# Optimization experiments

Measured on AMD Instinct MI355X. Metric: run time of the kernel, lower is better.

Reference implementation:

```python
import jax, jax.numpy as jnp
import numpy as np

NUM_HEADS = 12
KSIZE = 3
PAD = 1


def setup_inputs() -> dict:
    key = jax.random.key(0)
    ks = jax.random.split(key, 5)
    B, H, W, C = 4, 96, 96, 192
    x = jax.random.normal(ks[0], (B, H * W, C), jnp.float32)
    Wq = jax.random.normal(ks[1], (W, W), jnp.float32) * 0.02
    bq = jnp.zeros((W,), jnp.float32)
    Wkv = jax.random.normal(ks[2], (2 * W, W), jnp.float32) * 0.02
    bkv = jnp.zeros((2 * W,), jnp.float32)
    Wp = jax.random.normal(ks[3], (C, C), jnp.float32) * 0.02
    bp = jnp.zeros((C,), jnp.float32)
    f_qr = jnp.float32(1.0)
    f_kr = jnp.float32(1.0)
    f_vr = jnp.float32(1.0)
    return {"x": x, "Wq": Wq, "bq": bq, "Wkv": Wkv, "bkv": bkv, "Wp": Wp,
            "bp": bp, "f_qr": f_qr, "f_kr": f_kr, "f_vr": f_vr, "H": H, "W": W}


def reference(x, Wq, bq, Wkv, bkv, Wp, bp, f_qr, f_kr, f_vr, H, W):
    B, N, C = x.shape
    nh = NUM_HEADS
    hc = C // nh
    scale = C ** (-0.5)
    # faithful to torch: raw reshape of (B, N, C) into (B, C, H, W)
    xn = x.reshape(B, C, H, W)
    # q_proj is Linear over the last (width) axis, size Hw == W
    q = jnp.einsum('bchw,vw->bchv', xn, Wq) + bq            # (B,C,H,W)
    q = q.reshape(B, H, W, nh, hc).transpose(0, 3, 1, 2, 4)  # (B,nh,H,W,hc)
    q = (q * scale * f_qr).reshape(B, nh, H * W, hc)         # (B,nh,L,hc)
    # kv_proj: Linear(W -> 2W) over last axis
    kv = jnp.einsum('bchw,vw->bchv', xn, Wkv) + bkv          # (B,C,H,2W)
    kv = kv.reshape(B, H, W, 2, nh, hc).transpose(3, 0, 4, 5, 1, 2)  # (2,B,nh,hc,H,W)
    kv = jnp.pad(kv, ((0, 0),) * 4 + ((PAD, PAD), (PAD, PAD)))       # zero-pad spatial
    # unfold: 3x3 sliding windows, stride 1 -> one window per pixel
    patches = jnp.stack([kv[..., i:i + H, j:j + W]
                         for i in range(KSIZE) for j in range(KSIZE)], axis=4)
    # (2,B,nh,hc,9,H,W) -> (2,B,nh,L,9,hc); kernel index = kh*3+kw matches nn.Unfold
    patches = patches.reshape(2, B, nh, hc, KSIZE * KSIZE, H * W).transpose(0, 1, 2, 5, 4, 3)
    k = patches[0] * f_kr                                    # (B,nh,L,9,hc)
    v = patches[1] * f_vr
    attn = jax.nn.softmax(jnp.einsum('bnlc,bnlkc->bnlk', q, k), axis=-1)  # (B,nh,L,9)
    out = jnp.einsum('bnlk,bnlkc->bnlc', attn, v)            # (B,nh,L,hc)
    out = out.transpose(0, 2, 1, 3).reshape(B, H, W, C)      # (B,H,W,C)
    out = jnp.einsum('bhwc,oc->bhwo', out, Wp) + bp          # proj Linear(dim,dim)
    return out.reshape(B, H * W, C)
```

## Files before the change

kernel.cpp:

```cpp
#include <hip/hip_runtime.h>

#define HW2   96
#define NH    12
#define LPIX  (HW2*HW2)
#define BATCH 4

typedef __attribute__((ext_vector_type(8))) short bf16x8;
typedef __attribute__((ext_vector_type(4))) float f32x4;

static __device__ __forceinline__ float bf2f(unsigned short u) {
  union { unsigned int i; float f; } v; v.i = ((unsigned int)u) << 16; return v.f;
}
static __device__ __forceinline__ unsigned short f2bf(float f) {
  union { float f; unsigned int i; } v; v.f = f;
  unsigned int r = v.i + 0x7FFF + ((v.i >> 16) & 1);
  return (unsigned short)(r >> 16);
}

__global__ __launch_bounds__(256) void cvt_w_kernel(
    const float* __restrict__ Wq, const float* __restrict__ Wkv,
    const float* __restrict__ Wp,
    unsigned short* __restrict__ wqb, unsigned short* __restrict__ wkvb,
    unsigned short* __restrict__ wpb) {
  int i = blockIdx.x * 256 + threadIdx.x;
  if (i < 9216)       wqb[i]          = f2bf(Wq[i]);
  else if (i < 27648) wkvb[i - 9216]  = f2bf(Wkv[i - 9216]);
  else if (i < 64512) wpb[i - 27648]  = f2bf(Wp[i - 27648]);
}

__global__ __launch_bounds__(256) void qkv_gemm(
    const float* __restrict__ X,
    const unsigned short* __restrict__ wq, const unsigned short* __restrict__ wkv,
    const float* __restrict__ bq, const float* __restrict__ bkv,
    const float* __restrict__ fqr, const float* __restrict__ fkr,
    const float* __restrict__ fvr,
    unsigned short* __restrict__ Qb, unsigned short* __restrict__ KVb)
{
  __shared__ unsigned short lds[19456];
  unsigned short* xs  = lds;
  unsigned short* qo  = lds;
  unsigned short* kvo = lds + 6656;

  const int tid = threadIdx.x;
  const int r0  = blockIdx.x * 64;

  const float4* xsrc = (const float4*)(X + (size_t)r0 * 96);
  #pragma unroll
  for (int it = 0; it < 6; it++) {
    int c = tid + it * 256;
    float4 v = xsrc[c];
    int row = c / 24, col = (c % 24) * 4;
    ushort4 p;
    p.x = f2bf(v.x); p.y = f2bf(v.y); p.z = f2bf(v.z); p.w = f2bf(v.w);
    *(ushort4*)&xs[row * 120 + col] = p;
  }
  __syncthreads();

  const int lane = tid & 63, w = tid >> 6;
  const int col  = lane & 15;
  const int koff = (lane >> 4) * 8;
  const int arow = 16 * w + (lane & 15);
  const int rloc = 16 * w + 4 * (lane >> 4);

  bf16x8 af0 = *(const bf16x8*)&xs[arow * 120 + koff];
  bf16x8 af1 = *(const bf16x8*)&xs[arow * 120 + koff + 32];
  bf16x8 af2 = *(const bf16x8*)&xs[arow * 120 + koff + 64];
  __syncthreads();

  const float fqr0 = fqr[0] * 0.07216878364870322f;
  const float fkr0 = fkr[0], fvr0 = fvr[0];

  #pragma unroll
  for (int nt = 0; nt < 18; nt++) {
    const unsigned short* wrow = (nt < 6)
        ? wq  + (size_t)(nt * 16 + col) * 96 + koff
        : wkv + (size_t)((nt - 6) * 16 + col) * 96 + koff;
    bf16x8 b0 = *(const bf16x8*)(wrow);
    bf16x8 b1 = *(const bf16x8*)(wrow + 32);
    bf16x8 b2 = *(const bf16x8*)(wrow + 64);
    f32x4 acc = {0.f, 0.f, 0.f, 0.f};
    acc = __builtin_amdgcn_mfma_f32_16x16x32_bf16(af0, b0, acc, 0, 0, 0);
    acc = __builtin_amdgcn_mfma_f32_16x16x32_bf16(af1, b1, acc, 0, 0, 0);
    acc = __builtin_amdgcn_mfma_f32_16x16x32_bf16(af2, b2, acc, 0, 0, 0);

    if (nt < 6) {
      int u = nt * 16 + col;
      float bias = bq[u];
      #pragma unroll
      for (int i = 0; i < 4; i++)
        qo[(rloc + i) * 104 + u] = f2bf((acc[i] + bias) * fqr0);
    } else {
      int u = (nt - 6) * 16 + col;
      float bias = bkv[u];
      #pragma unroll
      for (int i = 0; i < 4; i++) {
        float s = (i & 1) ? fvr0 : fkr0;
        kvo[(rloc + i) * 200 + u] = f2bf((acc[i] + bias) * s);
      }
    }
  }
  __syncthreads();

  #pragma unroll
  for (int it = 0; it < 3; it++) {
    int c = tid + it * 256;
    int row = c / 12, cc = (c % 12) * 8;
    *(bf16x8*)(Qb + (size_t)(r0 + row) * 96 + cc) = *(const bf16x8*)&qo[row * 104 + cc];
  }
  #pragma unroll
  for (int it = 0; it < 6; it++) {
    int c = tid + it * 256;
    int row = c / 24, cc = (c % 24) * 8;
    *(bf16x8*)(KVb + (size_t)(r0 + row) * 192 + cc) = *(const bf16x8*)&kvo[row * 200 + cc];
  }
}

__global__ __launch_bounds__(384) void attnproj_kernel(
    const unsigned short* __restrict__ Qb, const unsigned short* __restrict__ KVb,
    const unsigned short* __restrict__ wp, const float* __restrict__ bp,
    float* __restrict__ Out)
{
  __shared__ unsigned short s_out[32 * 200];
  const int tid = threadIdx.x;
  const int bl0 = blockIdx.x * 32;

  {
    const int n  = tid % NH;
    const int pl = tid / NH;
    const int bl = bl0 + pl;
    const int l  = bl % LPIX;
    const int b  = bl / LPIX;
    const int h2 = l / HW2, w2 = l - h2 * HW2;

    const unsigned short* qp = Qb + (size_t)bl * 192 + n * 16;
    uint4 qA = *(const uint4*)(qp);
    uint4 qB = *(const uint4*)(qp + 8);

    const unsigned short* kvb = KVb + (size_t)b * (LPIX * 384) + n * 16;

    int  nbo[9];
    bool okk[9];
    uint4 kA[9], kB[9];
    #pragma unroll
    for (int kk = 0; kk < 9; kk++) {
      int hh = h2 + kk / 3 - 1;
      int ww = w2 + kk % 3 - 1;
      okk[kk] = ((unsigned)hh < (unsigned)HW2) && ((unsigned)ww < (unsigned)HW2);
      int hc = min(max(hh, 0), HW2 - 1);
      int wc = min(max(ww, 0), HW2 - 1);
      nbo[kk] = (hc * HW2 + wc) * 384;
      const unsigned short* kp = kvb + nbo[kk];
      kA[kk] = *(const uint4*)(kp);
      kB[kk] = *(const uint4*)(kp + 8);
    }

    float q[16];
    {
      const unsigned short* qs = (const unsigned short*)&qA;
      #pragma unroll
      for (int j = 0; j < 8; j++) q[j] = bf2f(qs[j]);
      qs = (const unsigned short*)&qB;
      #pragma unroll
      for (int j = 0; j < 8; j++) q[8 + j] = bf2f(qs[j]);
    }

    float sc[9];
    #pragma unroll
    for (int kk = 0; kk < 9; kk++) {
      float s = 0.f;
      const unsigned short* kd = (const unsigned short*)&kA[kk];
      #pragma unroll
      for (int j = 0; j < 8; j++) s = fmaf(q[j], bf2f(kd[j]), s);
      kd = (const unsigned short*)&kB[kk];
      #pragma unroll
      for (int j = 0; j < 8; j++) s = fmaf(q[8 + j], bf2f(kd[j]), s);
      sc[kk] = okk[kk] ? s : 0.f;
    }

    uint4 vA[9], vB[9];
    #pragma unroll
    for (int kk = 0; kk < 9; kk++) {
      const unsigned short* vp = kvb + nbo[kk] + 192;
      vA[kk] = *(const uint4*)(vp);
      vB[kk] = *(const uint4*)(vp + 8);
    }

    float m = sc[0];
    #pragma unroll
    for (int kk = 1; kk < 9; kk++) m = fmaxf(m, sc[kk]);
    float ssum = 0.f;
    #pragma unroll
    for (int kk = 0; kk < 9; kk++) {
      float e = __expf(sc[kk] - m);
      sc[kk] = e;
      ssum += e;
    }

    float acc[16];
    #pragma unroll
    for (int j = 0; j < 16; j++) acc[j] = 0.f;
    #pragma unroll
    for (int kk = 0; kk < 9; kk++) {
      float wgt = okk[kk] ? sc[kk] : 0.f;
      const unsigned short* vd = (const unsigned short*)&vA[kk];
      #pragma unroll
      for (int j = 0; j < 8; j++) acc[j] = fmaf(wgt, bf2f(vd[j]), acc[j]);
      vd = (const unsigned short*)&vB[kk];
      #pragma unroll
      for (int j = 0; j < 8; j++) acc[8 + j] = fmaf(wgt, bf2f(vd[j]), acc[8 + j]);
    }
    float rinv = 1.f / ssum;
    unsigned short od[16];
    #pragma unroll
    for (int j = 0; j < 16; j++) od[j] = f2bf(acc[j] * rinv);
    unsigned short* op = s_out + pl * 200 + n * 16;
    *(uint4*)(op)     = *(uint4*)&od[0];
    *(uint4*)(op + 8) = *(uint4*)&od[8];
  }
  __syncthreads();

  const int lane = tid & 63, w = tid >> 6;
  const int wr = w & 1, wh = w >> 1;
  const int col  = lane & 15;
  const int koff = (lane >> 4) * 8;
  const int arow = 16 * wr + (lane & 15);
  const int rbase = bl0 + 16 * wr + 4 * (lane >> 4);

  bf16x8 af[6];
  #pragma unroll
  for (int kt = 0; kt < 6; kt++)
    af[kt] = *(const bf16x8*)&s_out[arow * 200 + koff + kt * 32];

  #pragma unroll
  for (int t4 = 0; t4 < 4; t4++) {
    int nt = wh * 4 + t4;
    const unsigned short* wrow = wp + (size_t)(nt * 16 + col) * 192 + koff;
    f32x4 acc = {0.f, 0.f, 0.f, 0.f};
    #pragma unroll
    for (int kt = 0; kt < 6; kt++) {
      bf16x8 bfr = *(const bf16x8*)(wrow + kt * 32);
      acc = __builtin_amdgcn_mfma_f32_16x16x32_bf16(af[kt], bfr, acc, 0, 0, 0);
    }
    int u = nt * 16 + col;
    float bias = bp[u];
    #pragma unroll
    for (int i = 0; i < 4; i++)
      Out[(size_t)(rbase + i) * 192 + u] = acc[i] + bias;
  }
}

extern "C" void kernel_launch(void* const* d_in, const int* in_sizes, int n_in,
                              void* d_out, int out_size, void* d_ws, size_t ws_size,
                              hipStream_t stream) {
  const float* x   = (const float*)d_in[0];
  const float* Wq  = (const float*)d_in[1];
  const float* bq  = (const float*)d_in[2];
  const float* Wkv = (const float*)d_in[3];
  const float* bkv = (const float*)d_in[4];
  const float* Wp  = (const float*)d_in[5];
  const float* bp  = (const float*)d_in[6];
  const float* fqr = (const float*)d_in[7];
  const float* fkr = (const float*)d_in[8];
  const float* fvr = (const float*)d_in[9];

  char* ws = (char*)d_ws;
  unsigned short* Qb   = (unsigned short*)ws;
  unsigned short* KVb  = (unsigned short*)(ws + 14155776);
  unsigned short* wqb  = (unsigned short*)(ws + 42467328);
  unsigned short* wkvb = (unsigned short*)(ws + 42485760);
  unsigned short* wpb  = (unsigned short*)(ws + 42522624);

  cvt_w_kernel<<<dim3(252), dim3(256), 0, stream>>>(Wq, Wkv, Wp, wqb, wkvb, wpb);

  qkv_gemm<<<dim3(1152), dim3(256), 0, stream>>>(
      x, wqb, wkvb, bq, bkv, fqr, fkr, fvr, Qb, KVb);

  attnproj_kernel<<<dim3(1152), dim3(384), 0, stream>>>(
      Qb, KVb, wpb, bp, (float*)d_out);
}
```

Before: 77.32 us.

## Store Q and KV head-major so attention gathers are contiguous per head

The QKV GEMM epilogue now writes Q and K/V into head-major buffers (batch, head, pixel, channels), with K and V for each pixel interleaved into 32-element rows. The attention kernel maps threads so the 32 pixels in a block share one head, which makes each 3x3 neighbour gather a short contiguous read within that head's plane instead of a 768-byte strided access across all heads. The LDS row stride for the projection input is padded to avoid bank conflicts. The cost is scattered 16-byte stores in the GEMM epilogue.

```diff
diff --git a/kernel.cpp b/kernel.cpp
--- a/kernel.cpp
+++ b/kernel.cpp
@@ -34,7 +34,7 @@
     const float* __restrict__ bq, const float* __restrict__ bkv,
     const float* __restrict__ fqr, const float* __restrict__ fkr,
     const float* __restrict__ fvr,
-    unsigned short* __restrict__ Qb, unsigned short* __restrict__ KVb)
+    unsigned short* __restrict__ Qh, unsigned short* __restrict__ KVh)
 {
   __shared__ unsigned short lds[19456];
   unsigned short* xs  = lds;
@@ -43,6 +43,8 @@
 
   const int tid = threadIdx.x;
   const int r0  = blockIdx.x * 64;
+  const int b   = r0 / 18432;
+  const int lb  = (r0 % 18432) >> 1;
 
   const float4* xsrc = (const float4*)(X + (size_t)r0 * 96);
   #pragma unroll
@@ -103,40 +105,52 @@
 
   #pragma unroll
   for (int it = 0; it < 3; it++) {
-    int c = tid + it * 256;
-    int row = c / 12, cc = (c % 12) * 8;
-    *(bf16x8*)(Qb + (size_t)(r0 + row) * 96 + cc) = *(const bf16x8*)&qo[row * 104 + cc];
+    int m = tid + it * 256;
+    int n = m >> 6, rem = m & 63;
+    int l_loc = rem >> 1, half = (m & 1) * 8;
+    int srow = 2 * l_loc + (n >= 6);
+    int scol = (n % 6) * 16 + half;
+    unsigned short* dst = Qh + (size_t)b * 1769472 + (size_t)n * 147456
+                        + (size_t)(lb + l_loc) * 16 + half;
+    *(uint4*)dst = *(const uint4*)&qo[srow * 104 + scol];
   }
   #pragma unroll
   for (int it = 0; it < 6; it++) {
-    int c = tid + it * 256;
-    int row = c / 24, cc = (c % 24) * 8;
-    *(bf16x8*)(KVb + (size_t)(r0 + row) * 192 + cc) = *(const bf16x8*)&kvo[row * 200 + cc];
+    int m = tid + it * 256;
+    int n = m >> 7, rem = m & 127;
+    int l_loc = rem >> 2;
+    int kv = (m >> 1) & 1, half = (m & 1) * 8;
+    int srow = 2 * l_loc + kv;
+    int scol = n * 16 + half;
+    unsigned short* dst = KVh + (size_t)b * 3538944 + (size_t)n * 294912
+                        + (size_t)(lb + l_loc) * 32 + kv * 16 + half;
+    *(uint4*)dst = *(const uint4*)&kvo[srow * 200 + scol];
   }
 }
 
 __global__ __launch_bounds__(384) void attnproj_kernel(
-    const unsigned short* __restrict__ Qb, const unsigned short* __restrict__ KVb,
+    const unsigned short* __restrict__ Qh, const unsigned short* __restrict__ KVh,
     const unsigned short* __restrict__ wp, const float* __restrict__ bp,
     float* __restrict__ Out)
 {
-  __shared__ unsigned short s_out[32 * 200];
+  __shared__ unsigned short s_out[32 * 204];
   const int tid = threadIdx.x;
   const int bl0 = blockIdx.x * 32;
 
   {
-    const int n  = tid % NH;
-    const int pl = tid / NH;
+    const int n  = tid >> 5;
+    const int pl = tid & 31;
     const int bl = bl0 + pl;
     const int l  = bl % LPIX;
     const int b  = bl / LPIX;
     const int h2 = l / HW2, w2 = l - h2 * HW2;
 
-    const unsigned short* qp = Qb + (size_t)bl * 192 + n * 16;
+    const unsigned short* qp = Qh + (size_t)b * 1769472 + (size_t)n * 147456
+                             + (size_t)l * 16;
     uint4 qA = *(const uint4*)(qp);
     uint4 qB = *(const uint4*)(qp + 8);
 
-    const unsigned short* kvb = KVb + (size_t)b * (LPIX * 384) + n * 16;
+    const unsigned short* kvb = KVh + (size_t)b * 3538944 + (size_t)n * 294912;
 
     int  nbo[9];
     bool okk[9];
@@ -148,7 +162,7 @@
       okk[kk] = ((unsigned)hh < (unsigned)HW2) && ((unsigned)ww < (unsigned)HW2);
       int hc = min(max(hh, 0), HW2 - 1);
       int wc = min(max(ww, 0), HW2 - 1);
-      nbo[kk] = (hc * HW2 + wc) * 384;
+      nbo[kk] = (hc * HW2 + wc) * 32;
       const unsigned short* kp = kvb + nbo[kk];
       kA[kk] = *(const uint4*)(kp);
       kB[kk] = *(const uint4*)(kp + 8);
@@ -180,7 +194,7 @@
     uint4 vA[9], vB[9];
     #pragma unroll
     for (int kk = 0; kk < 9; kk++) {
-      const unsigned short* vp = kvb + nbo[kk] + 192;
+      const unsigned short* vp = kvb + nbo[kk] + 16;
       vA[kk] = *(const uint4*)(vp);
       vB[kk] = *(const uint4*)(vp + 8);
     }
@@ -213,7 +227,7 @@
     unsigned short od[16];
     #pragma unroll
     for (int j = 0; j < 16; j++) od[j] = f2bf(acc[j] * rinv);
-    unsigned short* op = s_out + pl * 200 + n * 16;
+    unsigned short* op = s_out + pl * 204 + n * 16;
     *(uint4*)(op)     = *(uint4*)&od[0];
     *(uint4*)(op + 8) = *(uint4*)&od[8];
   }
@@ -229,7 +243,7 @@
   bf16x8 af[6];
   #pragma unroll
   for (int kt = 0; kt < 6; kt++)
-    af[kt] = *(const bf16x8*)&s_out[arow * 200 + koff + kt * 32];
+    af[kt] = *(const bf16x8*)&s_out[arow * 204 + koff + kt * 32];
 
   #pragma unroll
   for (int t4 = 0; t4 < 4; t4++) {
@@ -264,8 +278,8 @@
   const float* fvr = (const float*)d_in[9];
 
   char* ws = (char*)d_ws;
-  unsigned short* Qb   = (unsigned short*)ws;
-  unsigned short* KVb  = (unsigned short*)(ws + 14155776);
+  unsigned short* Qh   = (unsigned short*)ws;
+  unsigned short* KVh  = (unsigned short*)(ws + 14155776);
   unsigned short* wqb  = (unsigned short*)(ws + 42467328);
   unsigned short* wkvb = (unsigned short*)(ws + 42485760);
   unsigned short* wpb  = (unsigned short*)(ws + 42522624);
@@ -273,8 +287,8 @@
   cvt_w_kernel<<<dim3(252), dim3(256), 0, stream>>>(Wq, Wkv, Wp, wqb, wkvb, wpb);
 
   qkv_gemm<<<dim3(1152), dim3(256), 0, stream>>>(
-      x, wqb, wkvb, bq, bkv, fqr, fkr, fvr, Qb, KVb);
+      x, wqb, wkvb, bq, bkv, fqr, fkr, fvr, Qh, KVh);
 
   attnproj_kernel<<<dim3(1152), dim3(384), 0, stream>>>(
-      Qb, KVb, wpb, bp, (float*)d_out);
-}
+      Qh, KVh, wpb, bp, (float*)d_out);
+}
```

After: 90.35 us, median of 2. 16.8% more time.

## Batch global loads ahead of compute and swizzle block order in attention kernel

Applied to the files above, without the earlier changes.

Weight fragments in the QKV GEMM are loaded in groups of six tiles before their MFMAs, and the projection weights are all loaded before the projection MFMA loop, so more memory latency is in flight at once. In the attention kernel, V loads are issued together with K loads, ahead of the score computation. The LDS row stride is padded from 200 to 204 to reduce bank conflicts, and block indices are remapped across 8 groups to change the global memory access pattern. Launch-bounds occupancy hints are added to both kernels. The cost is higher register pressure, which could lower occupancy or cause spills.

```diff
diff --git a/kernel.cpp b/kernel.cpp
--- a/kernel.cpp
+++ b/kernel.cpp
@@ -28,7 +28,7 @@
   else if (i < 64512) wpb[i - 27648]  = f2bf(Wp[i - 27648]);
 }
 
-__global__ __launch_bounds__(256) void qkv_gemm(
+__global__ __launch_bounds__(256, 2) void qkv_gemm(
     const float* __restrict__ X,
     const unsigned short* __restrict__ wq, const unsigned short* __restrict__ wkv,
     const float* __restrict__ bq, const float* __restrict__ bkv,
@@ -71,31 +71,42 @@
   const float fkr0 = fkr[0], fvr0 = fvr[0];
 
   #pragma unroll
-  for (int nt = 0; nt < 18; nt++) {
-    const unsigned short* wrow = (nt < 6)
-        ? wq  + (size_t)(nt * 16 + col) * 96 + koff
-        : wkv + (size_t)((nt - 6) * 16 + col) * 96 + koff;
-    bf16x8 b0 = *(const bf16x8*)(wrow);
-    bf16x8 b1 = *(const bf16x8*)(wrow + 32);
-    bf16x8 b2 = *(const bf16x8*)(wrow + 64);
-    f32x4 acc = {0.f, 0.f, 0.f, 0.f};
-    acc = __builtin_amdgcn_mfma_f32_16x16x32_bf16(af0, b0, acc, 0, 0, 0);
-    acc = __builtin_amdgcn_mfma_f32_16x16x32_bf16(af1, b1, acc, 0, 0, 0);
-    acc = __builtin_amdgcn_mfma_f32_16x16x32_bf16(af2, b2, acc, 0, 0, 0);
-
-    if (nt < 6) {
-      int u = nt * 16 + col;
-      float bias = bq[u];
-      #pragma unroll
-      for (int i = 0; i < 4; i++)
-        qo[(rloc + i) * 104 + u] = f2bf((acc[i] + bias) * fqr0);
-    } else {
-      int u = (nt - 6) * 16 + col;
-      float bias = bkv[u];
-      #pragma unroll
-      for (int i = 0; i < 4; i++) {
-        float s = (i & 1) ? fvr0 : fkr0;
-        kvo[(rloc + i) * 200 + u] = f2bf((acc[i] + bias) * s);
+  for (int g = 0; g < 3; g++) {
+    bf16x8 bw0[6], bw1[6], bw2[6];
+    #pragma unroll
+    for (int j = 0; j < 6; j++) {
+      int nt = g * 6 + j;
+      const unsigned short* wrow = (nt < 6)
+          ? wq  + (size_t)(nt * 16 + col) * 96 + koff
+          : wkv + (size_t)((nt - 6) * 16 + col) * 96 + koff;
+      bw0[j] = *(const bf16x8*)(wrow);
+      bw1[j] = *(const bf16x8*)(wrow + 32);
+      bw2[j] = *(const bf16x8*)(wrow + 64);
+    }
+    asm volatile("" ::: "memory");
+
+    #pragma unroll
+    for (int j = 0; j < 6; j++) {
+      int nt = g * 6 + j;
+      f32x4 acc = {0.f, 0.f, 0.f, 0.f};
+      acc = __builtin_amdgcn_mfma_f32_16x16x32_bf16(af0, bw0[j], acc, 0, 0, 0);
+      acc = __builtin_amdgcn_mfma_f32_16x16x32_bf16(af1, bw1[j], acc, 0, 0, 0);
+      acc = __builtin_amdgcn_mfma_f32_16x16x32_bf16(af2, bw2[j], acc, 0, 0, 0);
+
+      if (nt < 6) {
+        int u = nt * 16 + col;
+        float bias = bq[u];
+        #pragma unroll
+        for (int i = 0; i < 4; i++)
+          qo[(rloc + i) * 104 + u] = f2bf((acc[i] + bias) * fqr0);
+      } else {
+        int u = (nt - 6) * 16 + col;
+        float bias = bkv[u];
+        #pragma unroll
+        for (int i = 0; i < 4; i++) {
+          float s = (i & 1) ? fvr0 : fkr0;
+          kvo[(rloc + i) * 200 + u] = f2bf((acc[i] + bias) * s);
+        }
       }
     }
   }
@@ -115,14 +126,15 @@
   }
 }
 
-__global__ __launch_bounds__(384) void attnproj_kernel(
+__global__ __launch_bounds__(384, 1) void attnproj_kernel(
     const unsigned short* __restrict__ Qb, const unsigned short* __restrict__ KVb,
     const unsigned short* __restrict__ wp, const float* __restrict__ bp,
     float* __restrict__ Out)
 {
-  __shared__ unsigned short s_out[32 * 200];
+  __shared__ unsigned short s_out[32 * 204];
   const int tid = threadIdx.x;
-  const int bl0 = blockIdx.x * 32;
+  const int bid = (blockIdx.x & 7) * 144 + (blockIdx.x >> 3);
+  const int bl0 = bid * 32;
 
   {
     const int n  = tid % NH;
@@ -140,7 +152,7 @@
 
     int  nbo[9];
     bool okk[9];
-    uint4 kA[9], kB[9];
+    uint4 kA[9], kB[9], vA[9], vB[9];
     #pragma unroll
     for (int kk = 0; kk < 9; kk++) {
       int hh = h2 + kk / 3 - 1;
@@ -153,6 +165,13 @@
       kA[kk] = *(const uint4*)(kp);
       kB[kk] = *(const uint4*)(kp + 8);
     }
+    #pragma unroll
+    for (int kk = 0; kk < 9; kk++) {
+      const unsigned short* vp = kvb + nbo[kk] + 192;
+      vA[kk] = *(const uint4*)(vp);
+      vB[kk] = *(const uint4*)(vp + 8);
+    }
+    asm volatile("" ::: "memory");
 
     float q[16];
     {
@@ -177,14 +196,6 @@
       sc[kk] = okk[kk] ? s : 0.f;
     }
 
-    uint4 vA[9], vB[9];
-    #pragma unroll
-    for (int kk = 0; kk < 9; kk++) {
-      const unsigned short* vp = kvb + nbo[kk] + 192;
-      vA[kk] = *(const uint4*)(vp);
-      vB[kk] = *(const uint4*)(vp + 8);
-    }
-
     float m = sc[0];
     #pragma unroll
     for (int kk = 1; kk < 9; kk++) m = fmaxf(m, sc[kk]);
@@ -213,7 +224,7 @@
     unsigned short od[16];
     #pragma unroll
     for (int j = 0; j < 16; j++) od[j] = f2bf(acc[j] * rinv);
-    unsigned short* op = s_out + pl * 200 + n * 16;
+    unsigned short* op = s_out + pl * 204 + n * 16;
     *(uint4*)(op)     = *(uint4*)&od[0];
     *(uint4*)(op + 8) = *(uint4*)&od[8];
   }
@@ -229,18 +240,26 @@
   bf16x8 af[6];
   #pragma unroll
   for (int kt = 0; kt < 6; kt++)
-    af[kt] = *(const bf16x8*)&s_out[arow * 200 + koff + kt * 32];
-
+    af[kt] = *(const bf16x8*)&s_out[arow * 204 + koff + kt * 32];
+
+  bf16x8 bw[4][6];
   #pragma unroll
   for (int t4 = 0; t4 < 4; t4++) {
     int nt = wh * 4 + t4;
     const unsigned short* wrow = wp + (size_t)(nt * 16 + col) * 192 + koff;
+    #pragma unroll
+    for (int kt = 0; kt < 6; kt++)
+      bw[t4][kt] = *(const bf16x8*)(wrow + kt * 32);
+  }
+  asm volatile("" ::: "memory");
+
+  #pragma unroll
+  for (int t4 = 0; t4 < 4; t4++) {
+    int nt = wh * 4 + t4;
     f32x4 acc = {0.f, 0.f, 0.f, 0.f};
     #pragma unroll
-    for (int kt = 0; kt < 6; kt++) {
-      bf16x8 bfr = *(const bf16x8*)(wrow + kt * 32);
-      acc = __builtin_amdgcn_mfma_f32_16x16x32_bf16(af[kt], bfr, acc, 0, 0, 0);
-    }
+    for (int kt = 0; kt < 6; kt++)
+      acc = __builtin_amdgcn_mfma_f32_16x16x32_bf16(af[kt], bw[t4][kt], acc, 0, 0, 0);
     int u = nt * 16 + col;
     float bias = bp[u];
     #pragma unroll
```

Result: faster. 73.51 us (-4.9%).
